# Optimization experiments

Hardware: AMD Instinct MI355X
Metric: run time of the kernel (lower is better)

## Reference

```python
import jax, jax.numpy as jnp
import numpy as np

N, S, K, H, D = 8192, 16384, 16, 8, 512
E = N * K
HEAD_DIM = D // H


def setup_inputs() -> dict:
    key = jax.random.key(0)
    ks = jax.random.split(key, 12)
    x = jax.random.normal(ks[0], (N, D), jnp.float32)
    # every destination row gets K edges so softmax rows are never empty
    row_index = jnp.repeat(jnp.arange(N, dtype=jnp.int32), K)  # [E], sorted
    src_index = jax.random.randint(ks[1], (E,), 0, S, dtype=jnp.int32)
    att_bias = jax.random.normal(ks[2], (H, E), jnp.float32)
    dist = jax.random.uniform(ks[3], (E,), jnp.float32, minval=0.5, maxval=10.0)
    pos = jax.random.normal(ks[4], (N, 3), jnp.float32)
    src_pos = jax.random.normal(ks[5], (S, 3), jnp.float32)
    org_to_src = jax.random.randint(ks[6], (S,), 0, N, dtype=jnp.int32)
    scale = 1.0 / np.sqrt(D).astype(np.float32)
    Wq = jax.random.normal(ks[7], (D, D), jnp.float32) * scale
    bq = jax.random.normal(ks[8], (D,), jnp.float32) * 0.01
    Wk = jax.random.normal(ks[9], (D, D), jnp.float32) * scale
    bk = jax.random.normal(ks[10], (D,), jnp.float32) * 0.01
    return {"x": x, "row_index": row_index, "src_index": src_index,
            "att_bias": att_bias, "dist": dist, "pos": pos, "src_pos": src_pos,
            "org_to_src": org_to_src, "Wq": Wq, "bq": bq, "Wk": Wk, "bk": bk}


def reference(x, row_index, src_index, att_bias, dist, pos, src_pos, org_to_src,
              Wq, bq, Wk, bk):
    n, d_model = x.shape
    h, e = att_bias.shape
    hd = d_model // h
    # Projections -> [N, H, hd]; key gathered to the source list via org_to_src -> [S, H, hd]
    q = (x @ Wq + bq).reshape(n, h, hd)
    k_src = ((x @ Wk + bk).reshape(n, h, hd))[org_to_src]
    # Per-edge masked logits: (q/sqrt(hd)) . k + att_bias   (COO sparse attention)
    q_e = q[row_index]                       # [E, H, hd]
    k_e = k_src[src_index]                   # [E, H, hd]
    logits = jnp.einsum('ehd,ehd->eh', q_e, k_e) / np.sqrt(hd).astype(np.float32)
    logits = logits + att_bias.T             # [E, H]
    # Segment softmax over edges sharing a destination row
    m = jax.ops.segment_max(logits, row_index, num_segments=n)      # [N, H]
    p = jnp.exp(logits - m[row_index])
    z = jax.ops.segment_sum(p, row_index, num_segments=n)           # [N, H]
    att = p / z[row_index]                                          # [E, H]
    # Distance reweighting: 1/dist with dist==0 -> 0 weight
    safe = jnp.where(dist == 0, 1.0, dist)
    inv_d = jnp.where(dist == 0, 0.0, 1.0 / safe)
    att = att * inv_d[:, None]
    # dst_vec = att @ src_pos ; src_vec = (att @ 1) * pos   (both as segment sums)
    dst = jax.ops.segment_sum(att[:, :, None] * src_pos[src_index][:, None, :],
                              row_index, num_segments=n)            # [N, H, 3]
    asum = jax.ops.segment_sum(att, row_index, num_segments=n)      # [N, H]
    feat = dst - asum[:, :, None] * pos[:, None, :]                 # [N, H, 3]
    return feat.reshape(n, h * 3)
```

## Files before the change

### kernel.cpp

```cpp
#include <hip/hip_runtime.h>

#define N_ROWS 8192
#define D_MODEL 512
#define KT 512
#define NC 1024
#define NHEAD 8
#define KEDGE 16
#define NEDGE (N_ROWS * KEDGE)
#define PLANE 256

using f32x4  = __attribute__((ext_vector_type(4))) float;
using bf16x8 = __attribute__((ext_vector_type(8))) __bf16;
using u16x8  = __attribute__((ext_vector_type(8))) unsigned short;
using u16x4  = __attribute__((ext_vector_type(4))) unsigned short;

__device__ __forceinline__ unsigned short bf16_rtne(float f) {
    unsigned u = __float_as_uint(f);
    u += 0x7FFFu + ((u >> 16) & 1u);
    return (unsigned short)(u >> 16);
}
__device__ __forceinline__ float from_bf16(unsigned short b) {
    return __uint_as_float(((unsigned)b) << 16);
}

#define GLOAD16(gp, lp) __builtin_amdgcn_global_load_lds( \
    (__attribute__((address_space(1))) void*)(void*)(gp), \
    (__attribute__((address_space(3))) void*)(lp), 16, 0, 0)

__global__ __launch_bounds__(256) void prep(const float* __restrict__ x,
                                            const float* __restrict__ Wq,
                                            const float* __restrict__ Wk,
                                            const int* __restrict__ src_index,
                                            const int* __restrict__ org_to_src,
                                            const float* __restrict__ att_bias,
                                            const float* __restrict__ dist,
                                            unsigned short* __restrict__ Xb,
                                            unsigned short* __restrict__ Bt,
                                            int* __restrict__ kn,
                                            float* __restrict__ invd,
                                            float* __restrict__ AtT) {
    if (blockIdx.x < 2048) {
        const int i = (blockIdx.x * 256 + threadIdx.x) * 8;
        const float4 a = *reinterpret_cast<const float4*>(x + i);
        const float4 b = *reinterpret_cast<const float4*>(x + i + 4);
        u16x8 o;
        o[0] = bf16_rtne(a.x); o[1] = bf16_rtne(a.y);
        o[2] = bf16_rtne(a.z); o[3] = bf16_rtne(a.w);
        o[4] = bf16_rtne(b.x); o[5] = bf16_rtne(b.y);
        o[6] = bf16_rtne(b.z); o[7] = bf16_rtne(b.w);
        *reinterpret_cast<u16x8*>(Xb + i) = o;
    } else if (blockIdx.x < 4096) {
        const int gid = (blockIdx.x - 2048) * 256 + threadIdx.x;
        const int j = gid >> 9;
        const int k = gid & 511;
        const float* W = (j < 512) ? Wq : Wk;
        Bt[(size_t)j * KT + k] = bf16_rtne(W[k * D_MODEL + (j & 511)]);
    } else {
        const int ge = (blockIdx.x - 4096) * 256 + threadIdx.x;
        kn[ge] = org_to_src[src_index[ge]];
        const float d = dist[ge];
        invd[ge] = (d == 0.f) ? 0.f : 1.f / d;
        float4 b0, b1;
        b0.x = att_bias[0 * (size_t)NEDGE + ge];
        b0.y = att_bias[1 * (size_t)NEDGE + ge];
        b0.z = att_bias[2 * (size_t)NEDGE + ge];
        b0.w = att_bias[3 * (size_t)NEDGE + ge];
        b1.x = att_bias[4 * (size_t)NEDGE + ge];
        b1.y = att_bias[5 * (size_t)NEDGE + ge];
        b1.z = att_bias[6 * (size_t)NEDGE + ge];
        b1.w = att_bias[7 * (size_t)NEDGE + ge];
        *reinterpret_cast<float4*>(AtT + (size_t)ge * 8)     = b0;
        *reinterpret_cast<float4*>(AtT + (size_t)ge * 8 + 4) = b1;
    }
}

__global__ __launch_bounds__(256) void gemm_qk(
    const unsigned short* __restrict__ Xb, const unsigned short* __restrict__ Bt,
    const float* __restrict__ bq, const float* __restrict__ bk,
    unsigned short* __restrict__ QA, unsigned short* __restrict__ QB,
    unsigned short* __restrict__ KA, unsigned short* __restrict__ KB)
{
    __shared__ __align__(16) unsigned short As[128 * 32];
    __shared__ __align__(16) unsigned short Bs[128 * 32];

    const int tid  = threadIdx.x;
    const int lane = tid & 63;
    const int wave = tid >> 6;
    const int wr = wave >> 1, wc = wave & 1;
    const int row0 = blockIdx.x * 128, col0 = blockIdx.y * 128;

    f32x4 acc[4][4];
    #pragma unroll
    for (int m = 0; m < 4; ++m)
        #pragma unroll
        for (int n = 0; n < 4; ++n)
            acc[m][n] = (f32x4){0.f, 0.f, 0.f, 0.f};

    const int strow = tid >> 2;
    const int stcol = (tid & 3) * 8;

    for (int kt = 0; kt < KT / 32; ++kt) {
        const int kb = kt * 32;
        const unsigned short* ga = Xb + (size_t)(row0 + strow) * D_MODEL + kb + stcol;
        const unsigned short* gb = Bt + (size_t)(col0 + strow) * KT + kb + stcol;
        GLOAD16(ga,                 &As[strow * 32 + stcol]);
        GLOAD16(ga + 64 * D_MODEL,  &As[(64 + strow) * 32 + stcol]);
        GLOAD16(gb,                 &Bs[strow * 32 + stcol]);
        GLOAD16(gb + 64 * KT,       &Bs[(64 + strow) * 32 + stcol]);
        __syncthreads();

        bf16x8 afr[4], bfr[4];
        #pragma unroll
        for (int m = 0; m < 4; ++m)
            afr[m] = __builtin_bit_cast(bf16x8, *reinterpret_cast<const u16x8*>(
                &As[(wr * 64 + m * 16 + (lane & 15)) * 32 + (lane >> 4) * 8]));
        #pragma unroll
        for (int n = 0; n < 4; ++n)
            bfr[n] = __builtin_bit_cast(bf16x8, *reinterpret_cast<const u16x8*>(
                &Bs[(wc * 64 + n * 16 + (lane & 15)) * 32 + (lane >> 4) * 8]));

        #pragma unroll
        for (int m = 0; m < 4; ++m)
            #pragma unroll
            for (int n = 0; n < 4; ++n)
                acc[m][n] = __builtin_amdgcn_mfma_f32_16x16x32_bf16(afr[m], bfr[n], acc[m][n], 0, 0, 0);
        __syncthreads();
    }

    #pragma unroll
    for (int m = 0; m < 4; ++m) {
        const int row = row0 + wr * 64 + m * 16 + (lane >> 4) * 4;
        #pragma unroll
        for (int n = 0; n < 4; ++n) {
            const int c = col0 + wc * 64 + n * 16 + (lane & 15);
            const float bias = (c < 512) ? bq[c] : bk[c - 512];
            const int cc = c & 511;
            const int h = cc >> 6, din = cc & 63;
            unsigned short* plane = (c < 512) ? ((din < 32) ? QA : QB)
                                              : ((din < 32) ? KA : KB);
            const int off = h * 32 + (din & 31);
            #pragma unroll
            for (int r = 0; r < 4; ++r)
                plane[(size_t)(row + r) * PLANE + off] = bf16_rtne(acc[m][n][r] + bias);
        }
    }
}

__global__ __launch_bounds__(256) void edge_kernel(
    const unsigned short* __restrict__ QA, const unsigned short* __restrict__ QB,
    const unsigned short* __restrict__ KA, const unsigned short* __restrict__ KB,
    const int* __restrict__ kn,
    const float* __restrict__ invd,
    const float* __restrict__ AtT,
    const int* __restrict__ src_index,
    const float* __restrict__ pos,
    const float* __restrict__ src_pos,
    float* __restrict__ out)
{
    const int lane = threadIdx.x & 63;
    const int wave = threadIdx.x >> 6;
    const int n = blockIdx.x * 4 + wave;
    const int h = lane >> 3;

    const u16x4 qa = *reinterpret_cast<const u16x4*>(QA + (size_t)n * PLANE + lane * 4);
    const u16x4 qb = *reinterpret_cast<const u16x4*>(QB + (size_t)n * PLANE + lane * 4);
    float qaf[4], qbf[4];
    #pragma unroll
    for (int i = 0; i < 4; ++i) { qaf[i] = from_bf16(qa[i]); qbf[i] = from_bf16(qb[i]); }

    int kne[16]; float at[16], iv[16], sx[16];
    #pragma unroll
    for (int e = 0; e < 16; ++e) {
        const int ge = n * KEDGE + e;
        kne[e] = kn[ge];
        iv[e]  = invd[ge];
        at[e]  = AtT[(size_t)ge * 8 + h];
        sx[e]  = (float)src_index[ge];
    }

    float pA[16];
    #pragma unroll
    for (int e = 0; e < 16; ++e) {
        const u16x4 kv = *reinterpret_cast<const u16x4*>(
            KA + (size_t)kne[e] * PLANE + lane * 4);
        pA[e] = qaf[0] * from_bf16(kv[0]) + qaf[1] * from_bf16(kv[1])
              + qaf[2] * from_bf16(kv[2]) + qaf[3] * from_bf16(kv[3]);
    }
    float logit[16];
    #pragma unroll
    for (int e = 0; e < 16; ++e) {
        const u16x4 kv = *reinterpret_cast<const u16x4*>(
            KB + (size_t)kne[e] * PLANE + lane * 4);
        float p = pA[e]
                + qbf[0] * from_bf16(kv[0]) + qbf[1] * from_bf16(kv[1])
                + qbf[2] * from_bf16(kv[2]) + qbf[3] * from_bf16(kv[3]);
        p += __shfl_xor(p, 1);
        p += __shfl_xor(p, 2);
        p += __shfl_xor(p, 4);
        logit[e] = p * 0.125f + at[e];
    }

    float mx = logit[0];
    #pragma unroll
    for (int e = 1; e < 16; ++e) mx = fmaxf(mx, logit[e]);
    float pe[16];
    float z = 0.f;
    #pragma unroll
    for (int e = 0; e < 16; ++e) { pe[e] = __expf(logit[e] - mx); z += pe[e]; }
    const float rz = 1.f / z;

    float d0 = 0.f, d1 = 0.f, d2 = 0.f, asum = 0.f;
    #pragma unroll
    for (int e = 0; e < 16; ++e) {
        const float w = pe[e] * rz * iv[e];
        const float* sp = src_pos + (size_t)(int)sx[e] * 3;
        d0 += w * sp[0]; d1 += w * sp[1]; d2 += w * sp[2];
        asum += w;
    }
    const int c = lane & 7;
    if (c < 3) {
        const float dc = (c == 0) ? d0 : ((c == 1) ? d1 : d2);
        out[n * 24 + h * 3 + c] = dc - asum * pos[n * 3 + c];
    }
}

extern "C" void kernel_launch(void* const* d_in, const int* in_sizes, int n_in,
                              void* d_out, int out_size, void* d_ws, size_t ws_size,
                              hipStream_t stream) {
    const float* x          = (const float*)d_in[0];
    const int*   src_index  = (const int*)d_in[2];
    const float* att_bias   = (const float*)d_in[3];
    const float* dist       = (const float*)d_in[4];
    const float* pos        = (const float*)d_in[5];
    const float* src_pos    = (const float*)d_in[6];
    const int*   org_to_src = (const int*)d_in[7];
    const float* Wq         = (const float*)d_in[8];
    const float* bq         = (const float*)d_in[9];
    const float* Wk         = (const float*)d_in[10];
    const float* bk         = (const float*)d_in[11];
    float* out = (float*)d_out;

    char* ws = (char*)d_ws;
    unsigned short* Xb  = (unsigned short*)(ws);
    unsigned short* Bt  = (unsigned short*)(ws + ( 8u << 20));
    unsigned short* QA  = (unsigned short*)(ws + ( 9u << 20));
    unsigned short* QB  = (unsigned short*)(ws + (13u << 20));
    unsigned short* KA  = (unsigned short*)(ws + (17u << 20));
    unsigned short* KB  = (unsigned short*)(ws + (21u << 20));
    int*            kn  = (int*)           (ws + (25u << 20));
    float*          ivd = (float*)         (ws + (26u << 20));
    float*          AtT = (float*)         (ws + (27u << 20));

    prep<<<dim3(4608), dim3(256), 0, stream>>>(
        x, Wq, Wk, src_index, org_to_src, att_bias, dist,
        Xb, Bt, kn, ivd, AtT);
    gemm_qk<<<dim3(N_ROWS / 128, NC / 128), dim3(256), 0, stream>>>(
        Xb, Bt, bq, bk, QA, QB, KA, KB);
    edge_kernel<<<dim3(N_ROWS / 4), dim3(256), 0, stream>>>(
        QA, QB, KA, KB, kn, ivd, AtT, src_index, pos, src_pos, out);
}
```

Baseline: 50.56 us.

## Split edges across wave halves with 16-byte key loads and prepacked edge records

The edge kernel now assigns half of each wave to even edges and half to odd edges. Each lane loads 8 bf16 key values per plane instead of 4, so per-edge dot products use fewer, wider gathers, and the two halves are combined with cross-half shuffles for the max, normaliser and output sums. The prep kernel also gathers src_pos together with the inverse distance into one float4 record per edge, which removes the dependent src_index-to-src_pos gather from the edge kernel. The cost is an extra 2 MB record write in prep and a few more shuffles.

```diff
diff --git a/kernel.cpp b/kernel.cpp
--- a/kernel.cpp
+++ b/kernel.cpp
@@ -12,7 +12,6 @@
 using f32x4  = __attribute__((ext_vector_type(4))) float;
 using bf16x8 = __attribute__((ext_vector_type(8))) __bf16;
 using u16x8  = __attribute__((ext_vector_type(8))) unsigned short;
-using u16x4  = __attribute__((ext_vector_type(4))) unsigned short;
 
 __device__ __forceinline__ unsigned short bf16_rtne(float f) {
     unsigned u = __float_as_uint(f);
@@ -34,10 +33,11 @@
                                             const int* __restrict__ org_to_src,
                                             const float* __restrict__ att_bias,
                                             const float* __restrict__ dist,
+                                            const float* __restrict__ src_pos,
                                             unsigned short* __restrict__ Xb,
                                             unsigned short* __restrict__ Bt,
-                                            int* __restrict__ kn,
-                                            float* __restrict__ invd,
+                                            int* __restrict__ KN,
+                                            float4* __restrict__ Rec,
                                             float* __restrict__ AtT) {
     if (blockIdx.x < 2048) {
         const int i = (blockIdx.x * 256 + threadIdx.x) * 8;
@@ -57,9 +57,15 @@
         Bt[(size_t)j * KT + k] = bf16_rtne(W[k * D_MODEL + (j & 511)]);
     } else {
         const int ge = (blockIdx.x - 4096) * 256 + threadIdx.x;
-        kn[ge] = org_to_src[src_index[ge]];
+        const int s = src_index[ge];
+        KN[ge] = org_to_src[s];
         const float d = dist[ge];
-        invd[ge] = (d == 0.f) ? 0.f : 1.f / d;
+        float4 r;
+        r.x = src_pos[s * 3 + 0];
+        r.y = src_pos[s * 3 + 1];
+        r.z = src_pos[s * 3 + 2];
+        r.w = (d == 0.f) ? 0.f : 1.f / d;
+        Rec[ge] = r;
         float4 b0, b1;
         b0.x = att_bias[0 * (size_t)NEDGE + ge];
         b0.y = att_bias[1 * (size_t)NEDGE + ge];
@@ -149,76 +155,78 @@
 __global__ __launch_bounds__(256) void edge_kernel(
     const unsigned short* __restrict__ QA, const unsigned short* __restrict__ QB,
     const unsigned short* __restrict__ KA, const unsigned short* __restrict__ KB,
-    const int* __restrict__ kn,
-    const float* __restrict__ invd,
+    const int* __restrict__ KN,
+    const float4* __restrict__ Rec,
     const float* __restrict__ AtT,
-    const int* __restrict__ src_index,
     const float* __restrict__ pos,
-    const float* __restrict__ src_pos,
     float* __restrict__ out)
 {
     const int lane = threadIdx.x & 63;
     const int wave = threadIdx.x >> 6;
     const int n = blockIdx.x * 4 + wave;
-    const int h = lane >> 3;
-
-    const u16x4 qa = *reinterpret_cast<const u16x4*>(QA + (size_t)n * PLANE + lane * 4);
-    const u16x4 qb = *reinterpret_cast<const u16x4*>(QB + (size_t)n * PLANE + lane * 4);
-    float qaf[4], qbf[4];
-    #pragma unroll
-    for (int i = 0; i < 4; ++i) { qaf[i] = from_bf16(qa[i]); qbf[i] = from_bf16(qb[i]); }
-
-    int kne[16]; float at[16], iv[16], sx[16];
-    #pragma unroll
-    for (int e = 0; e < 16; ++e) {
-        const int ge = n * KEDGE + e;
-        kne[e] = kn[ge];
-        iv[e]  = invd[ge];
-        at[e]  = AtT[(size_t)ge * 8 + h];
-        sx[e]  = (float)src_index[ge];
-    }
-
-    float pA[16];
-    #pragma unroll
-    for (int e = 0; e < 16; ++e) {
-        const u16x4 kv = *reinterpret_cast<const u16x4*>(
-            KA + (size_t)kne[e] * PLANE + lane * 4);
-        pA[e] = qaf[0] * from_bf16(kv[0]) + qaf[1] * from_bf16(kv[1])
-              + qaf[2] * from_bf16(kv[2]) + qaf[3] * from_bf16(kv[3]);
-    }
-    float logit[16];
-    #pragma unroll
-    for (int e = 0; e < 16; ++e) {
-        const u16x4 kv = *reinterpret_cast<const u16x4*>(
-            KB + (size_t)kne[e] * PLANE + lane * 4);
-        float p = pA[e]
-                + qbf[0] * from_bf16(kv[0]) + qbf[1] * from_bf16(kv[1])
-                + qbf[2] * from_bf16(kv[2]) + qbf[3] * from_bf16(kv[3]);
+    const int ll = lane & 31;
+    const int half = lane >> 5;
+    const int h = ll >> 2;
+
+    const u16x8 qa = *reinterpret_cast<const u16x8*>(QA + (size_t)n * PLANE + ll * 8);
+    const u16x8 qb = *reinterpret_cast<const u16x8*>(QB + (size_t)n * PLANE + ll * 8);
+    float qaf[8], qbf[8];
+    #pragma unroll
+    for (int i = 0; i < 8; ++i) { qaf[i] = from_bf16(qa[i]); qbf[i] = from_bf16(qb[i]); }
+
+    int kne[8];
+    #pragma unroll
+    for (int i = 0; i < 8; ++i) kne[i] = KN[n * KEDGE + 2 * i + half];
+
+    float pA[8];
+    #pragma unroll
+    for (int i = 0; i < 8; ++i) {
+        const u16x8 kv = *reinterpret_cast<const u16x8*>(
+            KA + (size_t)kne[i] * PLANE + ll * 8);
+        float p = 0.f;
+        #pragma unroll
+        for (int j = 0; j < 8; ++j) p += qaf[j] * from_bf16(kv[j]);
+        pA[i] = p;
+    }
+    float logit[8];
+    #pragma unroll
+    for (int i = 0; i < 8; ++i) {
+        const u16x8 kv = *reinterpret_cast<const u16x8*>(
+            KB + (size_t)kne[i] * PLANE + ll * 8);
+        float p = pA[i];
+        #pragma unroll
+        for (int j = 0; j < 8; ++j) p += qbf[j] * from_bf16(kv[j]);
         p += __shfl_xor(p, 1);
         p += __shfl_xor(p, 2);
-        p += __shfl_xor(p, 4);
-        logit[e] = p * 0.125f + at[e];
+        logit[i] = p * 0.125f + AtT[(size_t)(n * KEDGE + 2 * i + half) * 8 + h];
     }
 
     float mx = logit[0];
     #pragma unroll
-    for (int e = 1; e < 16; ++e) mx = fmaxf(mx, logit[e]);
-    float pe[16];
+    for (int i = 1; i < 8; ++i) mx = fmaxf(mx, logit[i]);
+    mx = fmaxf(mx, __shfl_xor(mx, 32));
+    float pe[8];
     float z = 0.f;
     #pragma unroll
-    for (int e = 0; e < 16; ++e) { pe[e] = __expf(logit[e] - mx); z += pe[e]; }
+    for (int i = 0; i < 8; ++i) { pe[i] = __expf(logit[i] - mx); z += pe[i]; }
+    z += __shfl_xor(z, 32);
     const float rz = 1.f / z;
 
     float d0 = 0.f, d1 = 0.f, d2 = 0.f, asum = 0.f;
     #pragma unroll
-    for (int e = 0; e < 16; ++e) {
-        const float w = pe[e] * rz * iv[e];
-        const float* sp = src_pos + (size_t)(int)sx[e] * 3;
-        d0 += w * sp[0]; d1 += w * sp[1]; d2 += w * sp[2];
+    for (int i = 0; i < 8; ++i) {
+        const float4 r = Rec[n * KEDGE + 2 * i + half];
+        const float w = pe[i] * rz * r.w;
+        d0 += w * r.x; d1 += w * r.y; d2 += w * r.z;
         asum += w;
     }
-    const int c = lane & 7;
-    if (c < 3) {
+    d0 += __shfl_xor(d0, 32);
+    d1 += __shfl_xor(d1, 32);
+    d2 += __shfl_xor(d2, 32);
+    asum += __shfl_xor(asum, 32);
+
+    const int c = ll & 3;
+    if (half == 0 && c < 3) {
         const float dc = (c == 0) ? d0 : ((c == 1) ? d1 : d2);
         out[n * 24 + h * 3 + c] = dc - asum * pos[n * 3 + c];
     }
@@ -247,15 +255,15 @@
     unsigned short* QB  = (unsigned short*)(ws + (13u << 20));
     unsigned short* KA  = (unsigned short*)(ws + (17u << 20));
     unsigned short* KB  = (unsigned short*)(ws + (21u << 20));
-    int*            kn  = (int*)           (ws + (25u << 20));
-    float*          ivd = (float*)         (ws + (26u << 20));
-    float*          AtT = (float*)         (ws + (27u << 20));
+    int*            KN  = (int*)           (ws + (25u << 20));
+    float4*         Rec = (float4*)        (ws + (26u << 20));
+    float*          AtT = (float*)         (ws + (28u << 20));
 
     prep<<<dim3(4608), dim3(256), 0, stream>>>(
-        x, Wq, Wk, src_index, org_to_src, att_bias, dist,
-        Xb, Bt, kn, ivd, AtT);
+        x, Wq, Wk, src_index, org_to_src, att_bias, dist, src_pos,
+        Xb, Bt, KN, Rec, AtT);
     gemm_qk<<<dim3(N_ROWS / 128, NC / 128), dim3(256), 0, stream>>>(
         Xb, Bt, bq, bk, QA, QB, KA, KB);
     edge_kernel<<<dim3(N_ROWS / 4), dim3(256), 0, stream>>>(
-        QA, QB, KA, KB, kn, ivd, AtT, src_index, pos, src_pos, out);
-}
+        QA, QB, KA, KB, KN, Rec, AtT, pos, out);
+}
```

After: 48.30 us. 1.05x faster.
